# Performance work log

Measured on AMD Instinct MI355X. Metric: run time of the kernel, lower is better.

The kernel has to match this reference:

```python
import jax, jax.numpy as jnp
import numpy as np


def setup_inputs() -> dict:
    key = jax.random.key(0)
    ks = jax.random.split(key, 8)
    H = 256  # hidden_size
    NH = 8   # num_heads
    HD = H // NH
    B, G = 256, 1024
    s = 1.0 / np.sqrt(H)
    return {
        "query": jax.random.normal(ks[0], (B, 2 * H), dtype=jnp.float32),
        "ref": jax.random.normal(ks[1], (B, G, H), dtype=jnp.float32),
        "Wq": jax.random.normal(ks[2], (H, 2 * H), dtype=jnp.float32) * s,
        "bq": jax.random.normal(ks[3], (H,), dtype=jnp.float32) * s,
        "We": jax.random.normal(ks[4], (H, H), dtype=jnp.float32) * s,
        "be": jax.random.normal(ks[5], (H,), dtype=jnp.float32) * s,
        "Wv": jax.random.normal(ks[6], (HD,), dtype=jnp.float32) * (1.0 / np.sqrt(HD)),
        "bv": jax.random.normal(ks[7], (1,), dtype=jnp.float32) * 0.01,
        "num_heads": 8,
    }


def reference(query, ref, Wq, bq, We, be, Wv, bv, num_heads):
    B, G, H = ref.shape
    hd = H // num_heads
    # q_dense: [B, 2H] -> [B, H] -> [B, nh, hd]
    q = (query @ Wq.T + bq).reshape(B, num_heads, hd)
    # e_dense: [B, G, H] -> [B, G, H] -> [B, G, nh, hd]
    e = (jnp.einsum('bgh,oh->bgo', ref, We) + be).reshape(B, G, num_heads, hd)
    # broadcast-add over graph dim, tanh, per-head linear scorer (hd -> 1)
    v = jnp.tanh(q[:, None, :, :] + e)                 # [B, G, nh, hd]
    s = jnp.einsum('bgnd,d->bgn', v, Wv) + bv[0]       # [B, G, nh]
    # sum over heads, output [B, 1, G] (matches sum(dim=1).transpose(1,2))
    return s.sum(axis=-1)[:, None, :]
```

## Files before the change

kernel.cpp:

```cpp
#include <hip/hip_runtime.h>

typedef __attribute__((ext_vector_type(8))) short short8;
typedef __attribute__((ext_vector_type(8))) unsigned short ushort8;
typedef __attribute__((ext_vector_type(4))) float f32x4;
typedef unsigned short ushort;
typedef unsigned int uint;

__device__ __forceinline__ ushort f2bf(float f) {
    uint x = __float_as_uint(f);
    x += 0x7fffu + ((x >> 16) & 1u);
    return (ushort)(x >> 16);
}

__global__ __launch_bounds__(256) void prep_q(
    const float* __restrict__ query, const float* __restrict__ Wq,
    const float* __restrict__ bq, const float* __restrict__ be,
    float* __restrict__ q_ws) {
    __shared__ float qrow[512];
    const int b = blockIdx.x, t = threadIdx.x;
    qrow[t]       = query[b * 512 + t];
    qrow[t + 256] = query[b * 512 + 256 + t];
    __syncthreads();
    const f32x4* wr = (const f32x4*)(Wq + (size_t)t * 512);
    float s = 0.f;
#pragma unroll 8
    for (int j = 0; j < 128; ++j) {
        f32x4 w = wr[j];
        f32x4 q = *(const f32x4*)(qrow + 4 * j);
        s += w.x * q.x + w.y * q.y + w.z * q.z + w.w * q.w;
    }
    q_ws[b * 256 + t] = s + bq[t] + be[t];
}

__global__ __launch_bounds__(256) void conv_we(
    const float* __restrict__ We, ushort* __restrict__ Web) {
    const int i = (blockIdx.x * 256 + threadIdx.x) * 4;
    float4 v = *(const float4*)(We + i);
    ushort4 u;
    u.x = f2bf(v.x); u.y = f2bf(v.y); u.z = f2bf(v.z); u.w = f2bf(v.w);
    *(ushort4*)(Web + i) = u;
}

#define BM 64
#define BK 32
#define LDA 40
#define LDB 40

__global__ __launch_bounds__(256) void fused_gemm(
    const float* __restrict__ ref, const ushort* __restrict__ Web,
    const float* __restrict__ q_ws, const float* __restrict__ Wv,
    const float* __restrict__ bv, float* __restrict__ out) {
    __shared__ ushort Asm[BM * LDA];
    __shared__ ushort Bsm[256 * LDB];
    __shared__ float red[4][64];

    const int t = threadIdx.x;
    const int w = t >> 6;
    const int l = t & 63;
    const int quad = l >> 4;
    const int lr = l & 15;
    const size_t row0 = (size_t)blockIdx.x * BM;
    const int b = (int)(row0 >> 10);

    f32x4 acc[4][4];
#pragma unroll
    for (int i = 0; i < 4; ++i)
#pragma unroll
        for (int j = 0; j < 4; ++j) acc[i][j] = (f32x4){0.f, 0.f, 0.f, 0.f};

    const int ar = t >> 2;
    const int ac = (t & 3) * 8;
    const float* aptr = ref + (row0 + ar) * 256 + ac;
    ushort* asd = Asm + ar * LDA + ac;

    const int br = t >> 2;
    const int bc = (t & 3) * 8;

    for (int kk = 0; kk < 8; ++kk) {
        float4 a0 = *(const float4*)(aptr + kk * 32);
        float4 a1 = *(const float4*)(aptr + kk * 32 + 4);
        ushort8 av;
        av[0] = f2bf(a0.x); av[1] = f2bf(a0.y); av[2] = f2bf(a0.z); av[3] = f2bf(a0.w);
        av[4] = f2bf(a1.x); av[5] = f2bf(a1.y); av[6] = f2bf(a1.z); av[7] = f2bf(a1.w);
        *(ushort8*)asd = av;
#pragma unroll
        for (int i = 0; i < 4; ++i) {
            const int n = br + i * 64;
            *(ushort8*)(Bsm + n * LDB + bc) =
                *(const ushort8*)(Web + n * 256 + kk * 32 + bc);
        }
        __syncthreads();

        short8 af[4], bf[4];
        const ushort* Ab = Asm + lr * LDA + quad * 8;
        const ushort* Bb = Bsm + (w * 64 + lr) * LDB + quad * 8;
#pragma unroll
        for (int rb = 0; rb < 4; ++rb) af[rb] = *(const short8*)(Ab + rb * 16 * LDA);
#pragma unroll
        for (int cb = 0; cb < 4; ++cb) bf[cb] = *(const short8*)(Bb + cb * 16 * LDB);
#pragma unroll
        for (int rb = 0; rb < 4; ++rb)
#pragma unroll
            for (int cb = 0; cb < 4; ++cb)
                acc[rb][cb] = __builtin_amdgcn_mfma_f32_16x16x32_bf16(
                    af[rb], bf[cb], acc[rb][cb], 0, 0, 0);
        __syncthreads();
    }

    const float* qe = q_ws + b * 256;
    const float wv0 = Wv[lr];
    const float wv1 = Wv[16 + lr];
    float qv[4];
#pragma unroll
    for (int cb = 0; cb < 4; ++cb) qv[cb] = qe[w * 64 + cb * 16 + lr];

    float part[4][4];
#pragma unroll
    for (int rb = 0; rb < 4; ++rb)
#pragma unroll
        for (int r = 0; r < 4; ++r) part[rb][r] = 0.f;

#pragma unroll
    for (int cb = 0; cb < 4; ++cb) {
        const float wvv = (cb & 1) ? wv1 : wv0;
#pragma unroll
        for (int rb = 0; rb < 4; ++rb)
#pragma unroll
            for (int r = 0; r < 4; ++r) {
                float x = acc[rb][cb][r] + qv[cb];
                float th = 1.f - 2.f / (__expf(2.f * x) + 1.f);
                part[rb][r] += th * wvv;
            }
    }
#pragma unroll
    for (int off = 1; off < 16; off <<= 1)
#pragma unroll
        for (int rb = 0; rb < 4; ++rb)
#pragma unroll
            for (int r = 0; r < 4; ++r)
                part[rb][r] += __shfl_xor(part[rb][r], off, 64);

    if (lr == 0) {
#pragma unroll
        for (int rb = 0; rb < 4; ++rb)
#pragma unroll
            for (int r = 0; r < 4; ++r)
                red[w][rb * 16 + quad * 4 + r] = part[rb][r];
    }
    __syncthreads();
    if (t < 64) {
        float s = red[0][t] + red[1][t] + red[2][t] + red[3][t] + 8.f * bv[0];
        out[row0 + t] = s;
    }
}

extern "C" void kernel_launch(void* const* d_in, const int* in_sizes, int n_in,
                              void* d_out, int out_size, void* d_ws, size_t ws_size,
                              hipStream_t stream) {
    const float* query = (const float*)d_in[0];
    const float* ref   = (const float*)d_in[1];
    const float* Wq    = (const float*)d_in[2];
    const float* bq    = (const float*)d_in[3];
    const float* We    = (const float*)d_in[4];
    const float* be    = (const float*)d_in[5];
    const float* Wv    = (const float*)d_in[6];
    const float* bv    = (const float*)d_in[7];
    float* out = (float*)d_out;

    float*  q_ws = (float*)d_ws;
    ushort* Web  = (ushort*)((char*)d_ws + 65536 * sizeof(float));

    prep_q<<<256, 256, 0, stream>>>(query, Wq, bq, be, q_ws);
    conv_we<<<64, 256, 0, stream>>>(We, Web);
    fused_gemm<<<4096, 256, 0, stream>>>(ref, Web, q_ws, Wv, bv, out);
}
```

Before: 432.9 us.

## Stage full A tile once in LDS, read B fragments from global, merge prep kernels

The GEMM kernel now loads and converts the whole 64x256 ref tile into LDS in a single phase with one barrier. The We fragments are read directly from global (L2-resident bf16) instead of being staged through LDS each k-step, which removes the per-iteration barriers. The two prep kernels are merged into one launch, and the q projection uses four independent accumulators. The trade-off is more LDS per block, no overlap between loading ref and the MFMA work, and B reads that go through cache instead of shared memory.

After: 441.8 us. 2.0% more time.

```diff
diff --git a/kernel.cpp b/kernel.cpp
--- a/kernel.cpp
+++ b/kernel.cpp
@@ -12,46 +12,50 @@
     return (ushort)(x >> 16);
 }
 
-__global__ __launch_bounds__(256) void prep_q(
+__global__ __launch_bounds__(256) void prep(
     const float* __restrict__ query, const float* __restrict__ Wq,
     const float* __restrict__ bq, const float* __restrict__ be,
-    float* __restrict__ q_ws) {
+    const float* __restrict__ We, float* __restrict__ q_ws,
+    ushort* __restrict__ Web) {
     __shared__ float qrow[512];
-    const int b = blockIdx.x, t = threadIdx.x;
+    const int t = threadIdx.x;
+    if (blockIdx.x < 64) {
+        const int i = (blockIdx.x * 256 + t) * 4;
+        float4 v = *(const float4*)(We + i);
+        ushort4 u;
+        u.x = f2bf(v.x); u.y = f2bf(v.y); u.z = f2bf(v.z); u.w = f2bf(v.w);
+        *(ushort4*)(Web + i) = u;
+        return;
+    }
+    const int b = blockIdx.x - 64;
     qrow[t]       = query[b * 512 + t];
     qrow[t + 256] = query[b * 512 + 256 + t];
     __syncthreads();
     const f32x4* wr = (const f32x4*)(Wq + (size_t)t * 512);
-    float s = 0.f;
-#pragma unroll 8
-    for (int j = 0; j < 128; ++j) {
-        f32x4 w = wr[j];
-        f32x4 q = *(const f32x4*)(qrow + 4 * j);
-        s += w.x * q.x + w.y * q.y + w.z * q.z + w.w * q.w;
+    float s0 = 0.f, s1 = 0.f, s2 = 0.f, s3 = 0.f;
+#pragma unroll 4
+    for (int j = 0; j < 128; j += 4) {
+        f32x4 w0 = wr[j], w1 = wr[j + 1], w2 = wr[j + 2], w3 = wr[j + 3];
+        f32x4 q0 = *(const f32x4*)(qrow + 4 * j);
+        f32x4 q1 = *(const f32x4*)(qrow + 4 * j + 4);
+        f32x4 q2 = *(const f32x4*)(qrow + 4 * j + 8);
+        f32x4 q3 = *(const f32x4*)(qrow + 4 * j + 12);
+        s0 += w0.x * q0.x + w0.y * q0.y + w0.z * q0.z + w0.w * q0.w;
+        s1 += w1.x * q1.x + w1.y * q1.y + w1.z * q1.z + w1.w * q1.w;
+        s2 += w2.x * q2.x + w2.y * q2.y + w2.z * q2.z + w2.w * q2.w;
+        s3 += w3.x * q3.x + w3.y * q3.y + w3.z * q3.z + w3.w * q3.w;
     }
-    q_ws[b * 256 + t] = s + bq[t] + be[t];
-}
-
-__global__ __launch_bounds__(256) void conv_we(
-    const float* __restrict__ We, ushort* __restrict__ Web) {
-    const int i = (blockIdx.x * 256 + threadIdx.x) * 4;
-    float4 v = *(const float4*)(We + i);
-    ushort4 u;
-    u.x = f2bf(v.x); u.y = f2bf(v.y); u.z = f2bf(v.z); u.w = f2bf(v.w);
-    *(ushort4*)(Web + i) = u;
+    q_ws[b * 256 + t] = (s0 + s1) + (s2 + s3) + bq[t] + be[t];
 }
 
 #define BM 64
-#define BK 32
-#define LDA 40
-#define LDB 40
+#define LDA 264
 
-__global__ __launch_bounds__(256) void fused_gemm(
+__global__ __launch_bounds__(256, 4) void fused_gemm(
     const float* __restrict__ ref, const ushort* __restrict__ Web,
     const float* __restrict__ q_ws, const float* __restrict__ Wv,
     const float* __restrict__ bv, float* __restrict__ out) {
     __shared__ ushort Asm[BM * LDA];
-    __shared__ ushort Bsm[256 * LDB];
     __shared__ float red[4][64];
 
     const int t = threadIdx.x;
@@ -62,49 +66,51 @@
     const size_t row0 = (size_t)blockIdx.x * BM;
     const int b = (int)(row0 >> 10);
 
+    {
+        const int row = t >> 2;
+        const int colbase = (t & 3) * 64;
+        const float4* ap = (const float4*)(ref + (row0 + row) * 256 + colbase);
+        ushort* as = Asm + row * LDA + colbase;
+#pragma unroll
+        for (int c = 0; c < 2; ++c) {
+            float4 buf[8];
+#pragma unroll
+            for (int j = 0; j < 8; ++j) buf[j] = ap[c * 8 + j];
+#pragma unroll
+            for (int j = 0; j < 4; ++j) {
+                float4 x = buf[2 * j], y = buf[2 * j + 1];
+                ushort8 v;
+                v[0] = f2bf(x.x); v[1] = f2bf(x.y); v[2] = f2bf(x.z); v[3] = f2bf(x.w);
+                v[4] = f2bf(y.x); v[5] = f2bf(y.y); v[6] = f2bf(y.z); v[7] = f2bf(y.w);
+                *(ushort8*)(as + c * 32 + j * 8) = v;
+            }
+        }
+    }
+    __syncthreads();
+
     f32x4 acc[4][4];
 #pragma unroll
     for (int i = 0; i < 4; ++i)
 #pragma unroll
         for (int j = 0; j < 4; ++j) acc[i][j] = (f32x4){0.f, 0.f, 0.f, 0.f};
 
-    const int ar = t >> 2;
-    const int ac = (t & 3) * 8;
-    const float* aptr = ref + (row0 + ar) * 256 + ac;
-    ushort* asd = Asm + ar * LDA + ac;
-
-    const int br = t >> 2;
-    const int bc = (t & 3) * 8;
-
-    for (int kk = 0; kk < 8; ++kk) {
-        float4 a0 = *(const float4*)(aptr + kk * 32);
-        float4 a1 = *(const float4*)(aptr + kk * 32 + 4);
-        ushort8 av;
-        av[0] = f2bf(a0.x); av[1] = f2bf(a0.y); av[2] = f2bf(a0.z); av[3] = f2bf(a0.w);
-        av[4] = f2bf(a1.x); av[5] = f2bf(a1.y); av[6] = f2bf(a1.z); av[7] = f2bf(a1.w);
-        *(ushort8*)asd = av;
+    const ushort* Bp = Web + ((size_t)(w * 64 + lr)) * 256 + quad * 8;
+    const ushort* Ap = Asm + lr * LDA + quad * 8;
+#pragma unroll 2
+    for (int k = 0; k < 8; ++k) {
+        short8 bfr[4], afr[4];
 #pragma unroll
-        for (int i = 0; i < 4; ++i) {
-            const int n = br + i * 64;
-            *(ushort8*)(Bsm + n * LDB + bc) =
-                *(const ushort8*)(Web + n * 256 + kk * 32 + bc);
-        }
-        __syncthreads();
-
-        short8 af[4], bf[4];
-        const ushort* Ab = Asm + lr * LDA + quad * 8;
-        const ushort* Bb = Bsm + (w * 64 + lr) * LDB + quad * 8;
+        for (int cb = 0; cb < 4; ++cb)
+            bfr[cb] = *(const short8*)(Bp + cb * 16 * 256 + k * 32);
 #pragma unroll
-        for (int rb = 0; rb < 4; ++rb) af[rb] = *(const short8*)(Ab + rb * 16 * LDA);
-#pragma unroll
-        for (int cb = 0; cb < 4; ++cb) bf[cb] = *(const short8*)(Bb + cb * 16 * LDB);
+        for (int rb = 0; rb < 4; ++rb)
+            afr[rb] = *(const short8*)(Ap + rb * 16 * LDA + k * 32);
 #pragma unroll
         for (int rb = 0; rb < 4; ++rb)
 #pragma unroll
             for (int cb = 0; cb < 4; ++cb)
                 acc[rb][cb] = __builtin_amdgcn_mfma_f32_16x16x32_bf16(
-                    af[rb], bf[cb], acc[rb][cb], 0, 0, 0);
-        __syncthreads();
+                    afr[rb], bfr[cb], acc[rb][cb], 0, 0, 0);
     }
 
     const float* qe = q_ws + b * 256;
@@ -170,7 +176,6 @@
     float*  q_ws = (float*)d_ws;
     ushort* Web  = (ushort*)((char*)d_ws + 65536 * sizeof(float));
 
-    prep_q<<<256, 256, 0, stream>>>(query, Wq, bq, be, q_ws);
-    conv_we<<<64, 256, 0, stream>>>(We, Web);
+    prep<<<320, 256, 0, stream>>>(query, Wq, bq, be, We, q_ws, Web);
     fused_gemm<<<4096, 256, 0, stream>>>(ref, Web, q_ws, Wv, bv, out);
 }
```
